# Kernel tuning notes

Hardware: AMD Instinct MI355X
Metric: run time of the kernel (lower is better)

## Reference

```python
import jax, jax.numpy as jnp
import numpy as np

NQ, NS, QN, SN = 10000, 500, 4, 10   # num_question, num_skill, q/s neighbor sizes
B, S, D = 32, 200, 128               # batch, seq_len, emb_dim
HOPS = 3


def setup_inputs() -> dict:
    key = jax.random.key(0)
    ks = iter(jax.random.split(key, 40))

    def nrm(shape, scale=0.05):
        return jax.random.normal(next(ks), shape, dtype=jnp.float32) * scale

    return {
        "question": jax.random.randint(next(ks), (B, S), 0, NQ),
        "response": jax.random.randint(next(ks), (B, S), 0, 2),
        "mask": jnp.ones((B, S), dtype=jnp.int32),
        "q_neighbors": jax.random.randint(next(ks), (NQ, QN), 0, NS),  # question -> skill ids
        "s_neighbors": jax.random.randint(next(ks), (NS, SN), 0, NQ),  # skill -> question ids
        "qs_skills": jax.random.randint(next(ks), (NQ, 4), 0, NS),     # related skills per question
        "emb_q": nrm((NQ, D), 1.0),
        "emb_s": nrm((NS, D), 1.0),
        "emb_r": nrm((2, D), 1.0),
        "W_ih": nrm((2 * D, 4 * D)), "b_ih": nrm((4 * D,)), "b_hh": nrm((4 * D,)),
        "ft_W": nrm((D, D)), "ft_b": nrm((D,)),
        "agg_W": nrm((HOPS, D, D)), "agg_b": nrm((HOPS, D)),
        "last_W": nrm((D, D)), "last_b": nrm((D,)),
        "q_W": nrm((D, D)), "q_b": nrm((D,)),
        "k_W": nrm((D, D)), "k_b": nrm((D,)),
        "w_W": nrm((2 * D,)), "w_b": nrm(()),
    }


def reference(question, response, mask, q_neighbors, s_neighbors, qs_skills,
              emb_q, emb_s, emb_r, W_ih, b_ih, b_hh, ft_W, ft_b,
              agg_W, agg_b, last_W, last_b, q_W, q_b, k_W, k_b, w_W, w_b):
    # ---- multi-hop GNN aggregation for every (b, t) question (mask == 1 everywhere) ----
    q_flat = question.reshape(-1)              # [B*S]
    lvl1 = q_neighbors[q_flat]                 # [N, QN]            skill ids
    lvl2 = s_neighbors[lvl1]                   # [N, QN, SN]        question ids
    lvl3 = q_neighbors[lvl2]                   # [N, QN, SN, QN]    skill ids
    embs = [emb_q[q_flat], emb_s[lvl1], emb_q[lvl2], emb_s[lvl3]]
    for i in range(HOPS):
        embs = [jnp.tanh((embs[j] + embs[j + 1].mean(axis=-2)) @ agg_W[j] + agg_b[j])
                for j in range(HOPS - i)]
    agg_emb = jnp.tanh(embs[0] @ last_W + last_b).reshape(B, S, D)

    # ---- per-step input + zero-state LSTMCell (source calls lstm_cell without hx) ----
    q_trans = jax.nn.relu(agg_emb @ ft_W + ft_b)
    x = jnp.concatenate([q_trans, emb_r[response]], axis=-1)   # [B, S, 2D]
    gates = x @ W_ih + b_ih + b_hh                             # h_prev = 0, c_prev = 0
    i_g, f_g, g_g, o_g = jnp.split(gates, 4, axis=-1)
    c = jax.nn.sigmoid(i_g) * jnp.tanh(g_g)
    h = jax.nn.sigmoid(o_g) * jnp.tanh(c)                      # [B, S, D]
    states = h[:, :S - 1]                                      # state written at step t

    # ---- soft-recap attention prediction for q_next = question[:, t+1] ----
    q_next = question[:, 1:]                                   # [B, T], T = S-1
    qs = jnp.concatenate([emb_q[q_next][:, :, None, :], emb_s[qs_skills[q_next]]], axis=2)  # [B,T,5,D]

    inner = jnp.einsum('bnd,btmd->btnm', states, qs)           # state/qs inner products
    a_state = (states @ q_W + q_b) @ w_W[:D]                   # [B, N]  MLP_query on states
    a_qs = (qs @ k_W + k_b) @ w_W[D:]                          # [B, T, 5] MLP_key on qs
    logits = a_state[:, None, :, None] + a_qs[:, :, None, :] + w_b  # [B, T, N, 5]

    t_idx = jnp.arange(S - 1)
    valid = t_idx[None, :] <= t_idx[:, None]                   # [T, N]: states 0..t visible at t
    logits = jnp.where(valid[None, :, :, None], logits, -jnp.inf)
    alpha = jax.nn.softmax(logits.reshape(B, S - 1, -1), axis=-1).reshape(logits.shape)
    pred = jnp.sum(alpha * jax.nn.sigmoid(inner), axis=(2, 3))  # [B, T]

    return jnp.zeros((B, S), jnp.float32).at[:, 1:].set(pred)
```

## Files before the change

kernel.cpp:

```cpp
#include <hip/hip_runtime.h>

typedef unsigned short u16;
typedef unsigned int   u32;

#define NQd 10000
#define NSd 500
#define Bd  32
#define Sd  200
#define Td  199
#define Dd  128
#define NR  6368
#define PB  208

typedef __attribute__((ext_vector_type(8))) short bf16x8;
typedef __attribute__((ext_vector_type(4))) float f32x4;

__device__ __forceinline__ float sigf(float x) {
  return __builtin_amdgcn_rcpf(1.f + __expf(-x));
}
__device__ __forceinline__ float tanh_f(float x) {
  float ax = fminf(fabsf(x), 15.f);
  float e = __expf(2.f * ax);
  float r = 1.f - 2.f * __builtin_amdgcn_rcpf(e + 1.f);
  return copysignf(r, x);
}
__device__ __forceinline__ float bf2f(u16 u) { return __uint_as_float(((u32)u) << 16); }
__device__ __forceinline__ u16 f2bf(float f) {
  u32 b = __float_as_uint(f);
  b += 0x7FFFu + ((b >> 16) & 1u);
  return (u16)(b >> 16);
}
__device__ __forceinline__ void unp2(u32 u, float &a, float &b) {
  a = __uint_as_float(u << 16);
  b = __uint_as_float(u & 0xffff0000u);
}
__device__ __forceinline__ void unpack16(uint4 a0, uint4 a1, float* f) {
  unp2(a0.x, f[0], f[1]);  unp2(a0.y, f[2], f[3]);
  unp2(a0.z, f[4], f[5]);  unp2(a0.w, f[6], f[7]);
  unp2(a1.x, f[8], f[9]);  unp2(a1.y, f[10], f[11]);
  unp2(a1.z, f[12], f[13]); unp2(a1.w, f[14], f[15]);
}

struct Args {
  const int *question, *response, *q_nb, *s_nb, *qs_sk;
  const float *emb_q, *emb_s, *emb_r;
  const float *W_ih, *b_ih, *b_hh, *ft_W, *ft_b, *agg_W, *agg_b, *last_W, *last_b;
  const float *q_W, *q_b, *k_W, *k_b, *w_W;
  u16 *tabA, *tabB, *tabs1, *tabs2, *states, *embq_bf, *embs_bf, *wts, *wiht;
  float *a_state, *qw, *kw, *scal, *er_part, *ev, *invZ, *pm;
  int *qid_map, *resp_map, *flag, *cnt, *list, *newidx;
};

struct WF { bf16x8 v[2][4]; };

__device__ __forceinline__ void load_WF(const u16* Wt, int l15, int quad, int cw, WF& w)
{
#pragma unroll
  for (int nt = 0; nt < 2; ++nt)
#pragma unroll
    for (int kc = 0; kc < 4; ++kc)
      w.v[nt][kc] = *(const bf16x8*)&Wt[(long)(cw + nt * 16 + l15) * 128 + kc * 32 + quad * 8];
}

__device__ __forceinline__ void zero_acc(f32x4 acc[2][2]) {
#pragma unroll
  for (int x = 0; x < 2; ++x)
#pragma unroll
    for (int y = 0; y < 2; ++y) acc[x][y] = (f32x4){0.f, 0.f, 0.f, 0.f};
}

__device__ __forceinline__ void mfma_WF(const u16* Al, const WF& w,
                                        int l15, int quad, f32x4 acc[2][2])
{
#pragma unroll
  for (int kc = 0; kc < 4; ++kc) {
    const int ko = kc * 32 + quad * 8;
    bf16x8 a0 = *(const bf16x8*)&Al[l15 * 136 + ko];
    bf16x8 a1 = *(const bf16x8*)&Al[(16 + l15) * 136 + ko];
    acc[0][0] = __builtin_amdgcn_mfma_f32_16x16x32_bf16(a0, w.v[0][kc], acc[0][0], 0, 0, 0);
    acc[0][1] = __builtin_amdgcn_mfma_f32_16x16x32_bf16(a0, w.v[1][kc], acc[0][1], 0, 0, 0);
    acc[1][0] = __builtin_amdgcn_mfma_f32_16x16x32_bf16(a1, w.v[0][kc], acc[1][0], 0, 0, 0);
    acc[1][1] = __builtin_amdgcn_mfma_f32_16x16x32_bf16(a1, w.v[1][kc], acc[1][1], 0, 0, 0);
  }
}

__device__ __forceinline__ void stage_A(const u16* Atab, const u16* Btab,
                                        const int* nbr, int K, const int* rowmap,
                                        int tile0, int rows, int tid, u16* Al)
{
  int r = tid & 31, k0 = (tid >> 5) * 16;
  int row = tile0 + r; if (row >= rows) row = rows - 1;
  int arow = rowmap ? rowmap[row] : row;
  const u16* ap = Atab + (long)arow * 128 + k0;
  if (K == 0) {
    *(uint4*)&Al[r * 136 + k0]     = *(const uint4*)ap;
    *(uint4*)&Al[r * 136 + k0 + 8] = *(const uint4*)(ap + 8);
  } else {
    float f[16];
    unpack16(*(const uint4*)ap, *(const uint4*)(ap + 8), f);
    float s[16];
#pragma unroll
    for (int q = 0; q < 16; ++q) s[q] = 0.f;
    for (int l = 0; l < K; ++l) {
      int id = nbr[(long)arow * K + l];
      const u16* np = Btab + (long)id * 128 + k0;
      float g[16];
      unpack16(*(const uint4*)np, *(const uint4*)(np + 8), g);
#pragma unroll
      for (int q = 0; q < 16; ++q) s[q] += g[q];
    }
    float inv = 1.f / (float)K;
#pragma unroll
    for (int q = 0; q < 16; ++q) f[q] += s[q] * inv;
    u32 p[8];
#pragma unroll
    for (int q = 0; q < 8; ++q)
      p[q] = (u32)f2bf(f[2 * q]) | ((u32)f2bf(f[2 * q + 1]) << 16);
    *(uint4*)&Al[r * 136 + k0]     = make_uint4(p[0], p[1], p[2], p[3]);
    *(uint4*)&Al[r * 136 + k0 + 8] = make_uint4(p[4], p[5], p[6], p[7]);
  }
}

__device__ __forceinline__ void update_A(const u16* Btab, const int* nbr,
                                         const int* rowmap, int tile0, int rows,
                                         int tid, u16* Al)
{
  int r = tid & 31, k0 = (tid >> 5) * 16;
  int row = tile0 + r; if (row >= rows) row = rows - 1;
  int arow = rowmap ? rowmap[row] : row;
  float f[16];
  unpack16(*(const uint4*)&Al[r * 136 + k0], *(const uint4*)&Al[r * 136 + k0 + 8], f);
  float s[16];
#pragma unroll
  for (int q = 0; q < 16; ++q) s[q] = 0.f;
#pragma unroll
  for (int l = 0; l < 4; ++l) {
    int id = nbr[(long)arow * 4 + l];
    const u16* np = Btab + (long)id * 128 + k0;
    float g[16];
    unpack16(*(const uint4*)np, *(const uint4*)(np + 8), g);
#pragma unroll
    for (int q = 0; q < 16; ++q) s[q] += g[q];
  }
#pragma unroll
  for (int q = 0; q < 16; ++q) f[q] += s[q] * 0.25f;
  u32 p[8];
#pragma unroll
  for (int q = 0; q < 8; ++q)
    p[q] = (u32)f2bf(f[2 * q]) | ((u32)f2bf(f[2 * q + 1]) << 16);
  *(uint4*)&Al[r * 136 + k0]     = make_uint4(p[0], p[1], p[2], p[3]);
  *(uint4*)&Al[r * 136 + k0 + 8] = make_uint4(p[4], p[5], p[6], p[7]);
}

__device__ __forceinline__ void epi_tanh_global(const f32x4 acc[2][2], const float* cbias,
                                                u16* out, int rows, int tile0,
                                                int l15, int quad, int cw)
{
#pragma unroll
  for (int nt = 0; nt < 2; ++nt) {
    int col = cw + nt * 16 + l15;
    float cb = cbias[col];
#pragma unroll
    for (int mt = 0; mt < 2; ++mt) {
      int rbase = tile0 + mt * 16 + quad * 4;
#pragma unroll
      for (int i = 0; i < 4; ++i) {
        int row = rbase + i;
        if (row >= rows) continue;
        out[(long)row * 128 + col] = f2bf(tanh_f(acc[mt][nt][i] + cb));
      }
    }
  }
}

__device__ __forceinline__ void epi_tanh_lds(const f32x4 acc[2][2], const float* cbias,
                                             u16* Al, int l15, int quad, int cw)
{
#pragma unroll
  for (int nt = 0; nt < 2; ++nt) {
    int col = cw + nt * 16 + l15;
    float cb = cbias[col];
#pragma unroll
    for (int mt = 0; mt < 2; ++mt)
#pragma unroll
      for (int i = 0; i < 4; ++i) {
        int rL = mt * 16 + quad * 4 + i;
        Al[rL * 136 + col] = f2bf(tanh_f(acc[mt][nt][i] + cb));
      }
  }
}

__global__ __launch_bounds__(256) void prep_all(Args a, float* __restrict__ out)
{
  const int T = gridDim.x * 256;
  for (int i = blockIdx.x * 256 + threadIdx.x; i < 497506; i += T) {
    if (i < 320000) {
      float4 v = *(const float4*)&a.emb_q[(long)i * 4];
      ((uint2*)a.embq_bf)[i] = make_uint2(
          (u32)f2bf(v.x) | ((u32)f2bf(v.y) << 16),
          (u32)f2bf(v.z) | ((u32)f2bf(v.w) << 16));
    } else if (i < 336000) {
      int c = i - 320000;
      float4 v = *(const float4*)&a.emb_s[(long)c * 4];
      ((uint2*)a.embs_bf)[c] = make_uint2(
          (u32)f2bf(v.x) | ((u32)f2bf(v.y) << 16),
          (u32)f2bf(v.z) | ((u32)f2bf(v.w) << 16));
    } else if (i < 417920) {
      int e = i - 336000;
      int seg = e >> 14, r = e & 16383;
      int col = r >> 7, k = r & 127;
      const float* src = (seg < 3) ? (a.agg_W + seg * 16384)
                                   : (seg == 3 ? a.last_W : a.ft_W);
      a.wts[e] = f2bf(src[k * 128 + col]);
    } else if (i < 483456) {
      int e = i - 417920;
      int col = e >> 7, k = e & 127;
      a.wiht[e] = f2bf(a.W_ih[k * 512 + col]);
    } else if (i < 489824) {
      int j = i - 483456;
      int b = j / Td, s = j - b * Td;
      int qid = a.question[b * Sd + s];
      a.qid_map[j]  = qid;
      a.resp_map[j] = a.response[b * Sd + s];
      if (atomicExch(&a.flag[qid], 1) == 0) {
        int idx = atomicAdd(a.cnt, 1);
        a.list[idx] = qid;
        a.newidx[qid] = idx;
      }
    } else if (i < 491106) {
      int s = i - 489824;
      if (s < 128) {
        float acc = 0;
        for (int e = 0; e < 128; ++e) acc += a.q_W[s * 128 + e] * a.w_W[e];
        a.qw[s] = acc;
      } else if (s < 256) {
        int d = s - 128; float acc = 0;
        for (int e = 0; e < 128; ++e) acc += a.k_W[d * 128 + e] * a.w_W[128 + e];
        a.kw[d] = acc;
      } else if (s == 256) {
        float acc = 0;
        for (int e = 0; e < 128; ++e) acc += a.q_b[e] * a.w_W[e];
        a.scal[0] = acc;
      } else if (s == 257) {
        float acc = 0;
        for (int e = 0; e < 128; ++e) acc += a.k_b[e] * a.w_W[128 + e];
        a.scal[1] = acc;
      } else {
        int e2 = s - 258, rr = e2 >> 9, col = e2 & 511;
        float acc = a.b_ih[col] + a.b_hh[col];
        for (int d = 0; d < 128; ++d) acc += a.emb_r[rr * Dd + d] * a.W_ih[(128 + d) * 512 + col];
        a.er_part[rr * 512 + col] = acc;
      }
    } else {
      out[i - 491106] = 0.f;
    }
  }
}

__global__ __launch_bounds__(256) void level1m(Args a)
{
  __shared__ __align__(16) u16 Al[32 * 136];
  const int i = blockIdx.x, tid = threadIdx.x;
  const int lane = tid & 63, wv = tid >> 6;
  const int l15 = lane & 15, quad = lane >> 4, cw = wv * 32;

  if (i >= 329) {
    int item = (i - 329) * 256 + tid;
    if (item >= NR) return;
    int b = item / Td, t = item - b * Td;
    int qn = a.question[b * Sd + t + 1];
    float am[5];
#pragma unroll
    for (int m = 0; m < 5; ++m) {
      const u16* src = (m == 0) ? a.embq_bf + (long)qn * 128
                                : a.embs_bf + (long)a.qs_sk[qn * 4 + (m - 1)] * 128;
      float s = 0.f;
      for (int k = 0; k < 128; k += 8) {
        uint4 u = *(const uint4*)&src[k];
        float f[8];
        unp2(u.x, f[0], f[1]); unp2(u.y, f[2], f[3]);
        unp2(u.z, f[4], f[5]); unp2(u.w, f[6], f[7]);
#pragma unroll
        for (int q = 0; q < 8; ++q) s = fmaf(f[q], a.kw[k + q], s);
      }
      am[m] = s + a.scal[1];
    }
    float mx = am[0];
#pragma unroll
    for (int m = 1; m < 5; ++m) mx = fmaxf(mx, am[m]);
    float ex[5], z = 0.f;
#pragma unroll
    for (int m = 0; m < 5; ++m) { ex[m] = __expf(am[m] - mx); z += ex[m]; }
    float iz = __builtin_amdgcn_rcpf(z);
#pragma unroll
    for (int m = 0; m < 5; ++m) a.pm[((long)b * PB + t) * 5 + m] = ex[m] * iz;
    return;
  }

  f32x4 acc[2][2];
  if (i >= 313) {
    const int tile0 = (i - 313) * 32;
    WF w1; load_WF(a.wts + 16384, l15, quad, cw, w1);
    stage_A(a.embs_bf, a.embq_bf, a.s_nb, 10, nullptr, tile0, NSd, tid, Al);
    __syncthreads();
    zero_acc(acc);
    mfma_WF(Al, w1, l15, quad, acc);
    epi_tanh_global(acc, a.agg_b + 128, a.tabs1, NSd, tile0, l15, quad, cw);
    return;
  }
  const int tile0 = i * 32;
  WF w2, w0;
  load_WF(a.wts + 2 * 16384, l15, quad, cw, w2);
  load_WF(a.wts, l15, quad, cw, w0);
  stage_A(a.embq_bf, a.embs_bf, a.q_nb, 4, nullptr, tile0, NQd, tid, Al);
  __syncthreads();
  zero_acc(acc);
  mfma_WF(Al, w2, l15, quad, acc);
  epi_tanh_global(acc, a.agg_b + 256, a.tabA, NQd, tile0, l15, quad, cw);
  zero_acc(acc);
  mfma_WF(Al, w0, l15, quad, acc);
  epi_tanh_global(acc, a.agg_b, a.tabB, NQd, tile0, l15, quad, cw);
}

__global__ __launch_bounds__(256) void g1k(Args a)
{
  __shared__ __align__(16) u16 Al[32 * 136];
  const int tid = threadIdx.x, tile0 = blockIdx.x * 32;
  const int lane = tid & 63, wv = tid >> 6;
  const int l15 = lane & 15, quad = lane >> 4, cw = wv * 32;
  WF w1; load_WF(a.wts + 16384, l15, quad, cw, w1);
  stage_A(a.tabs1, a.tabA, a.s_nb, 10, nullptr, tile0, NSd, tid, Al);
  __syncthreads();
  f32x4 acc[2][2];
  zero_acc(acc);
  mfma_WF(Al, w1, l15, quad, acc);
  epi_tanh_global(acc, a.agg_b + 128, a.tabs2, NSd, tile0, l15, quad, cw);
}

__global__ __launch_bounds__(256) void chain4(Args a)
{
  const int cnt = *a.cnt;
  const int tile0 = blockIdx.x * 32;
  if (tile0 >= cnt) return;
  __shared__ __align__(16) u16 Al[32 * 136];
  const int tid = threadIdx.x;
  const int lane = tid & 63, wv = tid >> 6;
  const int l15 = lane & 15, quad = lane >> 4, cw = wv * 32;
  WF w0, w3, w4;
  load_WF(a.wts, l15, quad, cw, w0);
  load_WF(a.wts + 3 * 16384, l15, quad, cw, w3);
  load_WF(a.wts + 4 * 16384, l15, quad, cw, w4);
  f32x4 acc[2][2];

  stage_A(a.tabB, a.tabs1, a.q_nb, 4, a.list, tile0, cnt, tid, Al);
  __syncthreads();
  zero_acc(acc);
  mfma_WF(Al, w0, l15, quad, acc);
  __syncthreads();
  epi_tanh_lds(acc, a.agg_b, Al, l15, quad, cw);
  __syncthreads();
  update_A(a.tabs2, a.q_nb, a.list, tile0, cnt, tid, Al);
  __syncthreads();
  zero_acc(acc);
  mfma_WF(Al, w0, l15, quad, acc);
  __syncthreads();
  epi_tanh_lds(acc, a.agg_b, Al, l15, quad, cw);
  __syncthreads();
  zero_acc(acc);
  mfma_WF(Al, w3, l15, quad, acc);
  __syncthreads();
  epi_tanh_lds(acc, a.last_b, Al, l15, quad, cw);
  __syncthreads();
  zero_acc(acc);
  mfma_WF(Al, w4, l15, quad, acc);
#pragma unroll
  for (int nt = 0; nt < 2; ++nt) {
    int col = cw + nt * 16 + l15;
    float cb = a.ft_b[col];
#pragma unroll
    for (int mt = 0; mt < 2; ++mt) {
      int rbase = tile0 + mt * 16 + quad * 4;
#pragma unroll
      for (int i = 0; i < 4; ++i) {
        int row = rbase + i;
        if (row >= cnt) continue;
        a.tabA[(long)row * 128 + col] = f2bf(fmaxf(acc[mt][nt][i] + cb, 0.f));
      }
    }
  }
}

__global__ __launch_bounds__(256) void gates_k(Args a)
{
  __shared__ __align__(16) u16 Al[32 * 136];
  __shared__ float hb[32 * 132];
  const int tid = threadIdx.x, tile0 = blockIdx.x * 32;
  const int lane = tid & 63, wv = tid >> 6;
  const int l15 = lane & 15, quad = lane >> 4, cw = wv * 32;
  WF wg0, wg1, wg2;
  load_WF(a.wiht, l15, quad, cw, wg0);
  load_WF(a.wiht + (long)256 * 128, l15, quad, cw, wg1);
  load_WF(a.wiht + (long)384 * 128, l15, quad, cw, wg2);
  {
    int r = tid & 31, k0 = (tid >> 5) * 16;
    int row = tile0 + r;
    int arow = a.newidx[a.qid_map[row]];
    const u16* ap = a.tabA + (long)arow * 128 + k0;
    *(uint4*)&Al[r * 136 + k0]     = *(const uint4*)ap;
    *(uint4*)&Al[r * 136 + k0 + 8] = *(const uint4*)(ap + 8);
  }
  __syncthreads();
  f32x4 acc[3][2][2];
  zero_acc(acc[0]); mfma_WF(Al, wg0, l15, quad, acc[0]);
  zero_acc(acc[1]); mfma_WF(Al, wg1, l15, quad, acc[1]);
  zero_acc(acc[2]); mfma_WF(Al, wg2, l15, quad, acc[2]);
#pragma unroll
  for (int nt = 0; nt < 2; ++nt) {
    int colL = cw + nt * 16 + l15;
#pragma unroll
    for (int mt = 0; mt < 2; ++mt) {
#pragma unroll
      for (int i = 0; i < 4; ++i) {
        int rL = mt * 16 + quad * 4 + i;
        int row = tile0 + rL;
        const float* rb = a.er_part + (long)a.resp_map[row] * 512;
        float iv = acc[0][mt][nt][i] + rb[colL];
        float gv = acc[1][mt][nt][i] + rb[256 + colL];
        float ov = acc[2][mt][nt][i] + rb[384 + colL];
        float c = sigf(iv) * tanh_f(gv);
        float h = sigf(ov) * tanh_f(c);
        a.states[(long)row * 128 + colL] = f2bf(h);
        hb[rL * 132 + colL] = h;
      }
    }
  }
  __syncthreads();
#pragma unroll
  for (int rr = 0; rr < 8; ++rr) {
    int rL = wv * 8 + rr;
    float p = hb[rL * 132 + lane] * a.qw[lane] + hb[rL * 132 + 64 + lane] * a.qw[64 + lane];
#pragma unroll
    for (int off = 32; off > 0; off >>= 1) p += __shfl_xor(p, off);
    if (lane == 0) a.a_state[tile0 + rL] = p + a.scal[0];
  }
}

__global__ __launch_bounds__(256) void bprep(Args a)
{
  __shared__ float red[256];
  __shared__ float evl[256];
  const int b = blockIdx.x, tid = threadIdx.x;
  float v = (tid < Td) ? a.a_state[b * Td + tid] : -1e30f;
  red[tid] = v; __syncthreads();
  for (int s = 128; s > 0; s >>= 1) { if (tid < s) red[tid] = fmaxf(red[tid], red[tid + s]); __syncthreads(); }
  float gmax = red[0];
  float e = (tid < Td) ? __expf(v - gmax) : 0.f;
  evl[tid] = e;
  if (tid < Td) a.ev[b * PB + tid] = e;
  __syncthreads();
  for (int off = 1; off < 256; off <<= 1) {
    float add = (tid >= off) ? evl[tid - off] : 0.f;
    __syncthreads();
    evl[tid] += add;
    __syncthreads();
  }
  if (tid < Td) a.invZ[b * PB + tid] = 1.f / evl[tid];
}

__global__ __launch_bounds__(256) void gk_pred(Args a, float* __restrict__ out)
{
  const int n0 = blockIdx.x * 32;
  const int c0 = blockIdx.y * 128;
  const int b  = blockIdx.z;
  int c_hi = c0 + 127; if (c_hi > 994) c_hi = 994;
  const int tmax = c_hi / 5, tmin = c0 / 5;
  if (n0 > tmax) return;

  __shared__ __align__(16) u16 smem[21760];
  __shared__ float predl[32];
  u16* Ql = smem;
  u16* Sl = smem + 17408;
  const int tid = threadIdx.x;
  if (tid < 32) predl[tid] = 0.f;
  {
    int r = tid & 31, k0 = (tid >> 5) * 16;
    int n = n0 + r; if (n > 198) n = 198;
    const u16* sp = a.states + ((long)b * Td + n) * 128 + k0;
    *(uint4*)&Sl[r * 136 + k0]     = *(const uint4*)sp;
    *(uint4*)&Sl[r * 136 + k0 + 8] = *(const uint4*)(sp + 8);
  }
  {
    int j = tid >> 1, k0 = (tid & 1) * 64;
    int col = c0 + j;
    uint4* dst = (uint4*)&Ql[j * 136 + k0];
    if (col < 995) {
      int t = col / 5, m = col - t * 5;
      int qn = a.question[b * Sd + t + 1];
      const u16* src = (m == 0) ? a.embq_bf + (long)qn * 128
                                : a.embs_bf + (long)a.qs_sk[qn * 4 + (m - 1)] * 128;
      src += k0;
#pragma unroll
      for (int q = 0; q < 8; ++q) dst[q] = ((const uint4*)src)[q];
    } else {
      uint4 z = make_uint4(0, 0, 0, 0);
#pragma unroll
      for (int q = 0; q < 8; ++q) dst[q] = z;
    }
  }
  __syncthreads();
  const int lane = tid & 63, wv = tid >> 6;
  const int l15 = lane & 15, quad = lane >> 4, cw = wv * 32;
  f32x4 acc[2][2];
  zero_acc(acc);
#pragma unroll
  for (int kc = 0; kc < 4; ++kc) {
    const int ko = kc * 32 + quad * 8;
    bf16x8 af[2], bfv[2];
    af[0]  = *(const bf16x8*)&Sl[l15 * 136 + ko];
    af[1]  = *(const bf16x8*)&Sl[(16 + l15) * 136 + ko];
    bfv[0] = *(const bf16x8*)&Ql[(cw + l15) * 136 + ko];
    bfv[1] = *(const bf16x8*)&Ql[(cw + 16 + l15) * 136 + ko];
#pragma unroll
    for (int mt = 0; mt < 2; ++mt)
#pragma unroll
      for (int nt = 0; nt < 2; ++nt)
        acc[mt][nt] = __builtin_amdgcn_mfma_f32_16x16x32_bf16(af[mt], bfv[nt], acc[mt][nt], 0, 0, 0);
  }

#pragma unroll
  for (int nt = 0; nt < 2; ++nt) {
    int col = c0 + cw + nt * 16 + l15;
    if (col >= 995) continue;
    int t = col / 5, m = col - t * 5;
    float pmv = a.pm[((long)b * PB + t) * 5 + m];
    float part = 0.f;
#pragma unroll
    for (int mt = 0; mt < 2; ++mt) {
      int nb = n0 + mt * 16 + quad * 4;
      if (nb > t) continue;
      float4 ev4 = *(const float4*)&a.ev[b * PB + nb];
      float evv[4] = {ev4.x, ev4.y, ev4.z, ev4.w};
#pragma unroll
      for (int i = 0; i < 4; ++i) {
        int n = nb + i;
        if (n > t || n > 198) continue;
        part += evv[i] * sigf(acc[mt][nt][i]);
      }
    }
    part *= pmv;
    if (part != 0.f) atomicAdd(&predl[t - tmin], part);
  }
  __syncthreads();
  const int tcnt = tmax - tmin + 1;
  if (tid < tcnt) {
    int t = tmin + tid;
    float pv = predl[tid];
    if (pv != 0.f)
      atomicAdd(&out[b * Sd + t + 1], pv * a.invZ[b * PB + t]);
  }
}

extern "C" void kernel_launch(void* const* d_in, const int* in_sizes, int n_in,
                              void* d_out, int out_size, void* d_ws, size_t ws_size,
                              hipStream_t stream)
{
  Args a;
  a.question = (const int*)d_in[0];
  a.response = (const int*)d_in[1];
  a.q_nb     = (const int*)d_in[3];
  a.s_nb     = (const int*)d_in[4];
  a.qs_sk    = (const int*)d_in[5];
  a.emb_q    = (const float*)d_in[6];
  a.emb_s    = (const float*)d_in[7];
  a.emb_r    = (const float*)d_in[8];
  a.W_ih     = (const float*)d_in[9];
  a.b_ih     = (const float*)d_in[10];
  a.b_hh     = (const float*)d_in[11];
  a.ft_W     = (const float*)d_in[12];
  a.ft_b     = (const float*)d_in[13];
  a.agg_W    = (const float*)d_in[14];
  a.agg_b    = (const float*)d_in[15];
  a.last_W   = (const float*)d_in[16];
  a.last_b   = (const float*)d_in[17];
  a.q_W      = (const float*)d_in[18];
  a.q_b      = (const float*)d_in[19];
  a.k_W      = (const float*)d_in[20];
  a.k_b      = (const float*)d_in[21];
  a.w_W      = (const float*)d_in[22];

  u16* wsu = (u16*)d_ws;
  const long NT = 1280000, ST = 64000, RT = (long)NR * Dd;
  a.tabA  = wsu;
  a.tabB  = a.tabA + NT;
  a.tabs1 = a.tabB + NT;
  a.tabs2 = a.tabs1 + ST;
  a.states  = a.tabs2 + ST;
  a.embq_bf = a.states + RT;
  a.embs_bf = a.embq_bf + NT;
  a.wts     = a.embs_bf + ST;
  a.wiht    = a.wts + 5 * 16384;
  float* fp = (float*)(a.wiht + 65536);
  a.a_state = fp;
  a.qw      = fp + 6368;
  a.kw      = fp + 6496;
  a.scal    = fp + 6624;
  a.er_part = fp + 6640;
  a.ev      = fp + 7664;
  a.invZ    = a.ev + 32 * PB;
  a.pm      = a.invZ + 32 * PB;
  a.qid_map  = (int*)(a.pm + 32 * PB * 5);
  a.resp_map = a.qid_map + NR;
  a.flag     = a.resp_map + NR;
  a.cnt      = a.flag + NQd;
  a.list     = a.cnt + 4;
  a.newidx   = a.list + NQd;

  float* out = (float*)d_out;

  hipMemsetAsync(a.flag, 0, (NQd + 4) * sizeof(int), stream);
  prep_all<<<640, 256, 0, stream>>>(a, out);
  level1m<<<354, 256, 0, stream>>>(a);
  g1k<<<16, 256, 0, stream>>>(a);
  chain4<<<199, 256, 0, stream>>>(a);
  gates_k<<<199, 256, 0, stream>>>(a);
  bprep<<<Bd, 256, 0, stream>>>(a);
  gk_pred<<<dim3(7, 8, Bd), 256, 0, stream>>>(a, out);
}
```

Baseline: 191.0 us.

## Merge prep and level-1 GNN kernels by reading fp32 inputs directly

The separate prep_all and level1m launches are merged into one kernel, prep2. Its level-1 aggregation blocks read the fp32 embeddings and agg_W directly, rounding to bf16 on the fly, so they no longer wait for the bf16 conversion pass. The softmax-over-keys (pm) computation moves from level1m into extra blocks of gates_k, which runs after embq_bf/embs_bf exist. This removes one kernel launch and one dependency barrier. In exchange, level-1 blocks do strided, uncoalesced fp32 weight loads and read twice as many bytes of embeddings.

```diff
diff --git a/kernel.cpp b/kernel.cpp
--- a/kernel.cpp
+++ b/kernel.cpp
@@ -30,6 +30,7 @@
   b += 0x7FFFu + ((b >> 16) & 1u);
   return (u16)(b >> 16);
 }
+__device__ __forceinline__ float rnd(float x) { return bf2f(f2bf(x)); }
 __device__ __forceinline__ void unp2(u32 u, float &a, float &b) {
   a = __uint_as_float(u << 16);
   b = __uint_as_float(u & 0xffff0000u);
@@ -60,6 +61,22 @@
 #pragma unroll
     for (int kc = 0; kc < 4; ++kc)
       w.v[nt][kc] = *(const bf16x8*)&Wt[(long)(cw + nt * 16 + l15) * 128 + kc * 32 + quad * 8];
+}
+
+__device__ __forceinline__ void load_WF_f32(const float* W, int l15, int quad, int cw, WF& w)
+{
+#pragma unroll
+  for (int nt = 0; nt < 2; ++nt) {
+    int col = cw + nt * 16 + l15;
+#pragma unroll
+    for (int kc = 0; kc < 4; ++kc) {
+      int kb = kc * 32 + quad * 8;
+      bf16x8 t;
+#pragma unroll
+      for (int j = 0; j < 8; ++j) t[j] = (short)f2bf(W[(long)(kb + j) * 128 + col]);
+      w.v[nt][kc] = t;
+    }
+  }
 }
 
 __device__ __forceinline__ void zero_acc(f32x4 acc[2][2]) {
@@ -121,6 +138,45 @@
   }
 }
 
+__device__ __forceinline__ void ld16_rnd(const float* p, float* f)
+{
+#pragma unroll
+  for (int q4 = 0; q4 < 4; ++q4) {
+    float4 v = *(const float4*)(p + q4 * 4);
+    f[q4 * 4 + 0] = rnd(v.x); f[q4 * 4 + 1] = rnd(v.y);
+    f[q4 * 4 + 2] = rnd(v.z); f[q4 * 4 + 3] = rnd(v.w);
+  }
+}
+
+__device__ __forceinline__ void stage_A_f32(const float* Atab, const float* Btab,
+                                            const int* nbr, int K,
+                                            int tile0, int rows, int tid, u16* Al)
+{
+  int r = tid & 31, k0 = (tid >> 5) * 16;
+  int row = tile0 + r; if (row >= rows) row = rows - 1;
+  float f[16];
+  ld16_rnd(Atab + (long)row * 128 + k0, f);
+  float s[16];
+#pragma unroll
+  for (int q = 0; q < 16; ++q) s[q] = 0.f;
+  for (int l = 0; l < K; ++l) {
+    int id = nbr[(long)row * K + l];
+    float g[16];
+    ld16_rnd(Btab + (long)id * 128 + k0, g);
+#pragma unroll
+    for (int q = 0; q < 16; ++q) s[q] += g[q];
+  }
+  float inv = 1.f / (float)K;
+#pragma unroll
+  for (int q = 0; q < 16; ++q) f[q] += s[q] * inv;
+  u32 p[8];
+#pragma unroll
+  for (int q = 0; q < 8; ++q)
+    p[q] = (u32)f2bf(f[2 * q]) | ((u32)f2bf(f[2 * q + 1]) << 16);
+  *(uint4*)&Al[r * 136 + k0]     = make_uint4(p[0], p[1], p[2], p[3]);
+  *(uint4*)&Al[r * 136 + k0 + 8] = make_uint4(p[4], p[5], p[6], p[7]);
+}
+
 __device__ __forceinline__ void update_A(const u16* Btab, const int* nbr,
                                          const int* rowmap, int tile0, int rows,
                                          int tid, u16* Al)
@@ -190,45 +246,79 @@
   }
 }
 
-__global__ __launch_bounds__(256) void prep_all(Args a, float* __restrict__ out)
-{
-  const int T = gridDim.x * 256;
-  for (int i = blockIdx.x * 256 + threadIdx.x; i < 497506; i += T) {
-    if (i < 320000) {
-      float4 v = *(const float4*)&a.emb_q[(long)i * 4];
-      ((uint2*)a.embq_bf)[i] = make_uint2(
+__global__ __launch_bounds__(256) void prep2(Args a, float* __restrict__ out)
+{
+  __shared__ __align__(16) u16 Al[32 * 136];
+  const int i = blockIdx.x, tid = threadIdx.x;
+  const int lane = tid & 63, wv = tid >> 6;
+  const int l15 = lane & 15, quad = lane >> 4, cw = wv * 32;
+
+  if (i < 313) {
+    const int tile0 = i * 32;
+    WF w2, w0;
+    load_WF_f32(a.agg_W + 2 * 16384, l15, quad, cw, w2);
+    load_WF_f32(a.agg_W, l15, quad, cw, w0);
+    stage_A_f32(a.emb_q, a.emb_s, a.q_nb, 4, tile0, NQd, tid, Al);
+    __syncthreads();
+    f32x4 acc[2][2];
+    zero_acc(acc);
+    mfma_WF(Al, w2, l15, quad, acc);
+    epi_tanh_global(acc, a.agg_b + 256, a.tabA, NQd, tile0, l15, quad, cw);
+    zero_acc(acc);
+    mfma_WF(Al, w0, l15, quad, acc);
+    epi_tanh_global(acc, a.agg_b, a.tabB, NQd, tile0, l15, quad, cw);
+    return;
+  }
+  if (i < 329) {
+    const int tile0 = (i - 313) * 32;
+    WF w1;
+    load_WF_f32(a.agg_W + 16384, l15, quad, cw, w1);
+    stage_A_f32(a.emb_s, a.emb_q, a.s_nb, 10, tile0, NSd, tid, Al);
+    __syncthreads();
+    f32x4 acc[2][2];
+    zero_acc(acc);
+    mfma_WF(Al, w1, l15, quad, acc);
+    epi_tanh_global(acc, a.agg_b + 128, a.tabs1, NSd, tile0, l15, quad, cw);
+    return;
+  }
+
+  const int T = 640 * 256;
+  for (int j = (i - 329) * 256 + tid; j < 497506; j += T) {
+    if (j < 320000) {
+      float4 v = *(const float4*)&a.emb_q[(long)j * 4];
+      ((uint2*)a.embq_bf)[j] = make_uint2(
           (u32)f2bf(v.x) | ((u32)f2bf(v.y) << 16),
           (u32)f2bf(v.z) | ((u32)f2bf(v.w) << 16));
-    } else if (i < 336000) {
-      int c = i - 320000;
+    } else if (j < 336000) {
+      int c = j - 320000;
       float4 v = *(const float4*)&a.emb_s[(long)c * 4];
       ((uint2*)a.embs_bf)[c] = make_uint2(
           (u32)f2bf(v.x) | ((u32)f2bf(v.y) << 16),
           (u32)f2bf(v.z) | ((u32)f2bf(v.w) << 16));
-    } else if (i < 417920) {
-      int e = i - 336000;
+    } else if (j < 417920) {
+      int e = j - 336000;
       int seg = e >> 14, r = e & 16383;
       int col = r >> 7, k = r & 127;
       const float* src = (seg < 3) ? (a.agg_W + seg * 16384)
                                    : (seg == 3 ? a.last_W : a.ft_W);
       a.wts[e] = f2bf(src[k * 128 + col]);
-    } else if (i < 483456) {
-      int e = i - 417920;
+    } else if (j < 483456) {
+      int e = j - 417920;
       int col = e >> 7, k = e & 127;
       a.wiht[e] = f2bf(a.W_ih[k * 512 + col]);
-    } else if (i < 489824) {
-      int j = i - 483456;
-      int b = j / Td, s = j - b * Td;
+    } else if (j < 489824) {
+      int jj = j - 483456;
+      int b = jj / Td, s = jj - b * Td;
       int qid = a.question[b * Sd + s];
-      a.qid_map[j]  = qid;
-      a.resp_map[j] = a.response[b * Sd + s];
+      a.qid_map[jj]  = qid;
+      a.resp_map[jj] = a.response[b * Sd + s];
       if (atomicExch(&a.flag[qid], 1) == 0) {
         int idx = atomicAdd(a.cnt, 1);
         a.list[idx] = qid;
         a.newidx[qid] = idx;
       }
-    } else if (i < 491106) {
-      int s = i - 489824;
+    } else if (j < 491106) {
+      int s = j - 489824;
       if (s < 128) {
         float acc = 0;
         for (int e = 0; e < 128; ++e) acc += a.q_W[s * 128 + e] * a.w_W[e];
@@ -252,74 +342,9 @@
         a.er_part[rr * 512 + col] = acc;
       }
     } else {
-      out[i - 491106] = 0.f;
-    }
-  }
-}
-
-__global__ __launch_bounds__(256) void level1m(Args a)
-{
-  __shared__ __align__(16) u16 Al[32 * 136];
-  const int i = blockIdx.x, tid = threadIdx.x;
-  const int lane = tid & 63, wv = tid >> 6;
-  const int l15 = lane & 15, quad = lane >> 4, cw = wv * 32;
-
-  if (i >= 329) {
-    int item = (i - 329) * 256 + tid;
-    if (item >= NR) return;
-    int b = item / Td, t = item - b * Td;
-    int qn = a.question[b * Sd + t + 1];
-    float am[5];
-#pragma unroll
-    for (int m = 0; m < 5; ++m) {
-      const u16* src = (m == 0) ? a.embq_bf + (long)qn * 128
-                                : a.embs_bf + (long)a.qs_sk[qn * 4 + (m - 1)] * 128;
-      float s = 0.f;
-      for (int k = 0; k < 128; k += 8) {
-        uint4 u = *(const uint4*)&src[k];
-        float f[8];
-        unp2(u.x, f[0], f[1]); unp2(u.y, f[2], f[3]);
-        unp2(u.z, f[4], f[5]); unp2(u.w, f[6], f[7]);
-#pragma unroll
-        for (int q = 0; q < 8; ++q) s = fmaf(f[q], a.kw[k + q], s);
-      }
-      am[m] = s + a.scal[1];
-    }
-    float mx = am[0];
-#pragma unroll
-    for (int m = 1; m < 5; ++m) mx = fmaxf(mx, am[m]);
-    float ex[5], z = 0.f;
-#pragma unroll
-    for (int m = 0; m < 5; ++m) { ex[m] = __expf(am[m] - mx); z += ex[m]; }
-    float iz = __builtin_amdgcn_rcpf(z);
-#pragma unroll
-    for (int m = 0; m < 5; ++m) a.pm[((long)b * PB + t) * 5 + m] = ex[m] * iz;
-    return;
-  }
-
-  f32x4 acc[2][2];
-  if (i >= 313) {
-    const int tile0 = (i - 313) * 32;
-    WF w1; load_WF(a.wts + 16384, l15, quad, cw, w1);
-    stage_A(a.embs_bf, a.embq_bf, a.s_nb, 10, nullptr, tile0, NSd, tid, Al);
-    __syncthreads();
-    zero_acc(acc);
-    mfma_WF(Al, w1, l15, quad, acc);
-    epi_tanh_global(acc, a.agg_b + 128, a.tabs1, NSd, tile0, l15, quad, cw);
-    return;
-  }
-  const int tile0 = i * 32;
-  WF w2, w0;
-  load_WF(a.wts + 2 * 16384, l15, quad, cw, w2);
-  load_WF(a.wts, l15, quad, cw, w0);
-  stage_A(a.embq_bf, a.embs_bf, a.q_nb, 4, nullptr, tile0, NQd, tid, Al);
-  __syncthreads();
-  zero_acc(acc);
-  mfma_WF(Al, w2, l15, quad, acc);
-  epi_tanh_global(acc, a.agg_b + 256, a.tabA, NQd, tile0, l15, quad, cw);
-  zero_acc(acc);
-  mfma_WF(Al, w0, l15, quad, acc);
-  epi_tanh_global(acc, a.agg_b, a.tabB, NQd, tile0, l15, quad, cw);
+      out[j - 491106] = 0.f;
+    }
+  }
 }
 
 __global__ __launch_bounds__(256) void g1k(Args a)
@@ -394,9 +419,44 @@
 {
   __shared__ __align__(16) u16 Al[32 * 136];
   __shared__ float hb[32 * 132];
-  const int tid = threadIdx.x, tile0 = blockIdx.x * 32;
+  const int tid = threadIdx.x;
   const int lane = tid & 63, wv = tid >> 6;
   const int l15 = lane & 15, quad = lane >> 4, cw = wv * 32;
+
+  if (blockIdx.x >= 199) {
+    int item = (blockIdx.x - 199) * 256 + tid;
+    if (item >= NR) return;
+    int b = item / Td, t = item - b * Td;
+    int qn = a.question[b * Sd + t + 1];
+    float am[5];
+#pragma unroll
+    for (int m = 0; m < 5; ++m) {
+      const u16* src = (m == 0) ? a.embq_bf + (long)qn * 128
+                                : a.embs_bf + (long)a.qs_sk[qn * 4 + (m - 1)] * 128;
+      float s = 0.f;
+      for (int k = 0; k < 128; k += 8) {
+        uint4 u = *(const uint4*)&src[k];
+        float f[8];
+        unp2(u.x, f[0], f[1]); unp2(u.y, f[2], f[3]);
+        unp2(u.z, f[4], f[5]); unp2(u.w, f[6], f[7]);
+#pragma unroll
+        for (int q = 0; q < 8; ++q) s = fmaf(f[q], a.kw[k + q], s);
+      }
+      am[m] = s + a.scal[1];
+    }
+    float mx = am[0];
+#pragma unroll
+    for (int m = 1; m < 5; ++m) mx = fmaxf(mx, am[m]);
+    float ex[5], z = 0.f;
+#pragma unroll
+    for (int m = 0; m < 5; ++m) { ex[m] = __expf(am[m] - mx); z += ex[m]; }
+    float iz = __builtin_amdgcn_rcpf(z);
+#pragma unroll
+    for (int m = 0; m < 5; ++m) a.pm[((long)b * PB + t) * 5 + m] = ex[m] * iz;
+    return;
+  }
+
+  const int tile0 = blockIdx.x * 32;
   WF wg0, wg1, wg2;
   load_WF(a.wiht, l15, quad, cw, wg0);
   load_WF(a.wiht + (long)256 * 128, l15, quad, cw, wg1);
@@ -618,11 +678,10 @@
   float* out = (float*)d_out;
 
   hipMemsetAsync(a.flag, 0, (NQd + 4) * sizeof(int), stream);
-  prep_all<<<640, 256, 0, stream>>>(a, out);
-  level1m<<<354, 256, 0, stream>>>(a);
+  prep2<<<969, 256, 0, stream>>>(a, out);
   g1k<<<16, 256, 0, stream>>>(a);
   chain4<<<199, 256, 0, stream>>>(a);
-  gates_k<<<199, 256, 0, stream>>>(a);
+  gates_k<<<224, 256, 0, stream>>>(a);
   bprep<<<Bd, 256, 0, stream>>>(a);
   gk_pred<<<dim3(7, 8, Bd), 256, 0, stream>>>(a, out);
 }
```

New measurement: 186.4 us. 2.4% less time.
